# Kernel tuning notes

Hardware: AMD Instinct MI355X
Metric: run time of the kernel (lower is better)

## Reference

```python
import jax, jax.numpy as jnp
import numpy as np

D_MODEL = 4096
D_LATENT = 512
NUM_HEADS = 32
HEAD_DIM = D_MODEL // NUM_HEADS  # 128
ROPE_THETA = 10000.0
BATCH, SEQ = 2, 2048


def _rotate_half(x):
    x1, x2 = jnp.split(x, 2, axis=-1)
    return jnp.concatenate([-x2, x1], axis=-1)


def _rope_cos_sin(positions, head_dim, theta, dtype):
    # positions: [B, S] -> cos/sin: [B, S, 1, head_dim]
    inv_freq = 1.0 / (theta ** (jnp.arange(0, head_dim, 2, dtype=jnp.float32) / head_dim))
    freqs = positions.astype(jnp.float32)[..., None] * inv_freq  # [B,S,hd/2]
    emb = jnp.concatenate([freqs, freqs], axis=-1)               # [B,S,hd]
    return jnp.cos(emb)[:, :, None, :].astype(dtype), jnp.sin(emb)[:, :, None, :].astype(dtype)


def setup_inputs() -> dict:
    key = jax.random.key(0)
    ks = jax.random.split(key, 6)
    s = 0.02
    return {
        "hidden_states": jax.random.normal(ks[0], (BATCH, SEQ, D_MODEL), jnp.float32),
        "Wq": jax.random.normal(ks[1], (D_MODEL, NUM_HEADS * HEAD_DIM), jnp.float32) * s,
        "Wc": jax.random.normal(ks[2], (D_MODEL, D_LATENT), jnp.float32) * s,
        "Wk": jax.random.normal(ks[3], (D_LATENT, NUM_HEADS * HEAD_DIM), jnp.float32) * s,
        "Wv": jax.random.normal(ks[4], (D_LATENT, NUM_HEADS * HEAD_DIM), jnp.float32) * s,
        "Wo": jax.random.normal(ks[5], (NUM_HEADS * HEAD_DIM, D_MODEL), jnp.float32) * s,
    }


def reference(hidden_states, Wq, Wc, Wk, Wv, Wo):
    B, S, _ = hidden_states.shape
    H, Dh = NUM_HEADS, HEAD_DIM

    q = (hidden_states @ Wq).reshape(B, S, H, Dh)
    kv_latent = hidden_states @ Wc                     # [B,S,d_latent]
    k = (kv_latent @ Wk).reshape(B, S, H, Dh)
    v = (kv_latent @ Wv).reshape(B, S, H, Dh)

    # RoPE: q uses positions [0..S), k uses positions [0..S) (no past cache)
    pos = jnp.broadcast_to(jnp.arange(S)[None, :], (B, S))
    cos, sin = _rope_cos_sin(pos, Dh, ROPE_THETA, q.dtype)
    q = q * cos + _rotate_half(q) * sin
    k = k * cos + _rotate_half(k) * sin

    # standard attention, no mask (faithful to attention_mask=None path)
    scale = 1.0 / np.sqrt(Dh)
    scores = jnp.einsum("bqhd,bkhd->bhqk", q, k) * scale
    probs = jax.nn.softmax(scores, axis=-1)
    attn = jnp.einsum("bhqk,bkhd->bqhd", probs, v)     # [B,S,H,Dh]

    out = attn.reshape(B, S, H * Dh) @ Wo
    return out
```

## Files before the change

kernel.cpp:

```cpp
#include <hip/hip_runtime.h>
#include <hip/hip_bf16.h>
#include <cstdint>
#include <cstddef>

#define D_MODEL 4096
#define D_LATENT 512
#define NUM_HEADS 32
#define HEAD_DIM 128
#define BATCH 2
#define SEQ 2048
#define ROWS (BATCH*SEQ)

typedef __attribute__((ext_vector_type(8))) short bf16x8;
typedef __attribute__((ext_vector_type(4))) float f32x4;
typedef __attribute__((ext_vector_type(16))) float f32x16;
typedef unsigned int uint;

static __device__ __forceinline__ unsigned short f2bf(float f){
  union { float f; uint32_t u; } v; v.f = f;
  uint32_t r = (v.u + 0x7fffu + ((v.u >> 16) & 1u)) >> 16;
  return (unsigned short)r;
}
static __device__ __forceinline__ float bf2f(unsigned short h){
  union { uint32_t u; float f; } v; v.u = ((uint32_t)h) << 16;
  return v.f;
}
static __device__ __forceinline__ uint cvtpk(float lo, float hi2){
  uint r;
  asm("v_cvt_pk_bf16_f32 %0, %1, %2" : "=v"(r) : "v"(lo), "v"(hi2));
  return r;
}
static __device__ __forceinline__ void gload16(const void* g, void* l){
  __builtin_amdgcn_global_load_lds(
      (const __attribute__((address_space(1))) void*)g,
      (__attribute__((address_space(3))) void*)l, 16, 0, 0);
}

__global__ __launch_bounds__(256) void f32_to_bf16(
    const float* __restrict__ in, unsigned short* __restrict__ out){
  const size_t i = ((size_t)blockIdx.x * 256 + threadIdx.x) * 8;
  const float4 lo = *(const float4*)(in + i);
  const float4 hi = *(const float4*)(in + i + 4);
  uint4 d; unsigned short* dp = (unsigned short*)&d;
  dp[0]=f2bf(lo.x); dp[1]=f2bf(lo.y); dp[2]=f2bf(lo.z); dp[3]=f2bf(lo.w);
  dp[4]=f2bf(hi.x); dp[5]=f2bf(hi.y); dp[6]=f2bf(hi.z); dp[7]=f2bf(hi.w);
  *(uint4*)(out + i) = d;
}

__global__ __launch_bounds__(256) void transpose_convert(
    const float* __restrict__ W, unsigned short* __restrict__ Wt, int K, int N){
  __shared__ float tile[64][65];
  const int k0 = blockIdx.x * 64, n0 = blockIdx.y * 64;
  const int t = threadIdx.x;
  #pragma unroll
  for (int j = 0; j < 16; ++j){
    const int idx = t + 256*j;
    const int r = idx >> 6, c = idx & 63;
    tile[r][c] = W[(size_t)(k0 + r) * N + n0 + c];
  }
  __syncthreads();
  #pragma unroll
  for (int j = 0; j < 16; ++j){
    const int idx = t + 256*j;
    const int r = idx >> 6, c = idx & 63;
    Wt[(size_t)(n0 + r) * K + k0 + c] = f2bf(tile[c][r]);
  }
}

__global__ __launch_bounds__(256) void v_transpose(
    const unsigned short* __restrict__ v, unsigned short* __restrict__ vt){
  __shared__ unsigned short tile[64][72];
  const int s0 = blockIdx.x * 64, d0 = blockIdx.y * 64, bh = blockIdx.z;
  const int b = bh >> 5, h = bh & 31;
  const int t = threadIdx.x;
  #pragma unroll
  for (int j = 0; j < 2; ++j){
    const int idx = t + 256*j;
    const int r = idx >> 3, ch = idx & 7;
    *(uint4*)&tile[r][ch*8] =
      *(const uint4*)&v[(size_t)(b*SEQ + s0 + r) * D_MODEL + h*128 + d0 + ch*8];
  }
  __syncthreads();
  #pragma unroll
  for (int j = 0; j < 16; ++j){
    const int idx = t + 256*j;
    const int r = idx >> 6, c = idx & 63;
    vt[((size_t)bh*128 + d0 + r) * SEQ + s0 + c] = tile[c][r];
  }
}

__global__ __launch_bounds__(256) void rope_table_kernel(float* __restrict__ ct,
                                                         float* __restrict__ st){
  const int i = blockIdx.x * 256 + threadIdx.x;
  if (i >= SEQ * 64) return;
  const int s = i >> 6, j = i & 63;
  const float inv = powf(10000.0f, -(float)j / 64.0f);
  const double a = (double)s * (double)inv;
  ct[i] = (float)cos(a);
  st[i] = (float)sin(a);
}

__global__ __launch_bounds__(256) void rope_apply(unsigned short* __restrict__ buf,
    const float* __restrict__ ct, const float* __restrict__ st, float scale){
  const int i = blockIdx.x * 256 + threadIdx.x;
  const int j = i & 63;
  const int tmp = i >> 6;
  const int h = tmp & 31;
  const int row = tmp >> 5;
  const int s = row & (SEQ - 1);
  const float c = ct[s*64 + j], sn = st[s*64 + j];
  const size_t base = (size_t)row * D_MODEL + (size_t)h * 128;
  const float x1 = bf2f(buf[base + j]);
  const float x2 = bf2f(buf[base + j + 64]);
  buf[base + j]      = f2bf((x1 * c - x2 * sn) * scale);
  buf[base + j + 64] = f2bf((x2 * c + x1 * sn) * scale);
}

template<bool OF32>
__global__ __launch_bounds__(256) void gemm_kernel(
    const unsigned short* __restrict__ A, const unsigned short* __restrict__ Bt,
    void* __restrict__ Cp, int M, int N, int K){
  __shared__ __align__(16) char As[128 * 128];
  __shared__ __align__(16) char Bs[128 * 128];
  const int t = threadIdx.x;
  const int m0 = blockIdx.y * 128, n0 = blockIdx.x * 128;
  const int l = t & 63, wid = t >> 6;
  const int wr = wid >> 1, wcn = wid & 1;
  const int lr = l & 15, lg = l >> 4;

  const int srow = l >> 3;
  const int gch  = (l & 7) ^ srow;
  const unsigned short* gA = A  + (size_t)(m0 + wid*32 + srow) * K + gch*8;
  const unsigned short* gB = Bt + (size_t)(n0 + wid*32 + srow) * K + gch*8;
  char* lA = As + wid*4096;
  char* lB = Bs + wid*4096;

  f32x4 acc[4][4];
  #pragma unroll
  for (int i = 0; i < 4; ++i)
    #pragma unroll
    for (int j = 0; j < 4; ++j)
      #pragma unroll
      for (int r = 0; r < 4; ++r) acc[i][j][r] = 0.0f;

  const int kTiles = K >> 6;
  for (int kt = 0; kt < kTiles; ++kt){
    const size_t ko = (size_t)kt << 6;
    #pragma unroll
    for (int i = 0; i < 4; ++i){
      gload16(gA + (size_t)i*8*K + ko, lA + i*1024);
      gload16(gB + (size_t)i*8*K + ko, lB + i*1024);
    }
    __syncthreads();
    #pragma unroll
    for (int kc = 0; kc < 2; ++kc){
      bf16x8 af[4], bfv[4];
      const int ch = kc*4 + lg;
      #pragma unroll
      for (int mb = 0; mb < 4; ++mb){
        const int row = wr*64 + mb*16 + lr;
        af[mb] = *(const bf16x8*)(As + row*128 + ((ch ^ (row & 7)) * 16));
      }
      #pragma unroll
      for (int nb = 0; nb < 4; ++nb){
        const int row = wcn*64 + nb*16 + lr;
        bfv[nb] = *(const bf16x8*)(Bs + row*128 + ((ch ^ (row & 7)) * 16));
      }
      #pragma unroll
      for (int mb = 0; mb < 4; ++mb)
        #pragma unroll
        for (int nb = 0; nb < 4; ++nb)
          acc[mb][nb] = __builtin_amdgcn_mfma_f32_16x16x32_bf16(af[mb], bfv[nb], acc[mb][nb], 0, 0, 0);
    }
    __syncthreads();
  }
  #pragma unroll
  for (int mb = 0; mb < 4; ++mb)
    #pragma unroll
    for (int nb = 0; nb < 4; ++nb)
      #pragma unroll
      for (int r = 0; r < 4; ++r){
        const int row = m0 + wr*64 + mb*16 + lg*4 + r;
        const int col = n0 + wcn*64 + nb*16 + lr;
        if constexpr (OF32) ((float*)Cp)[(size_t)row * N + col] = acc[mb][nb][r];
        else ((unsigned short*)Cp)[(size_t)row * N + col] = f2bf(acc[mb][nb][r]);
      }
}

template<int MH>
static __device__ __forceinline__ void rdAh(bf16x8 (&a_)[4][2], const char* buf,
                                            int wr, int lr, int lg){
  #pragma unroll
  for (int mm = 0; mm < 4; ++mm)
    #pragma unroll
    for (int kc = 0; kc < 2; ++kc){
      const int row = wr*128 + (MH*4 + mm)*16 + lr;
      const int ch = kc*4 + lg;
      a_[mm][kc] = *(const bf16x8*)(buf + row*128 + ((ch ^ (row & 7)) * 16));
    }
}
template<int NH>
static __device__ __forceinline__ void rdBh(bf16x8 (&b_)[2][2][2], const char* buf,
                                            int wc, int lr, int lg){
  #pragma unroll
  for (int nn = 0; nn < 2; ++nn)
    #pragma unroll
    for (int kc = 0; kc < 2; ++kc){
      const int row = wc*64 + (NH*2 + nn)*16 + lr;
      const int ch = kc*4 + lg;
      b_[NH][nn][kc] = *(const bf16x8*)(buf + row*128 + ((ch ^ (row & 7)) * 16));
    }
}
template<int MH, int NH>
static __device__ __forceinline__ void mfq(f32x4 (&acc)[8][4],
    const bf16x8 (&a_)[4][2], const bf16x8 (&b_)[2][2][2]){
  __builtin_amdgcn_s_setprio(1);
  #pragma unroll
  for (int kc = 0; kc < 2; ++kc)
    #pragma unroll
    for (int mm = 0; mm < 4; ++mm)
      #pragma unroll
      for (int nn = 0; nn < 2; ++nn)
        acc[MH*4+mm][NH*2+nn] = __builtin_amdgcn_mfma_f32_16x16x32_bf16(
            a_[mm][kc], b_[NH][nn][kc], acc[MH*4+mm][NH*2+nn], 0, 0, 0);
  __builtin_amdgcn_s_setprio(0);
}

#define G256_BAR  __builtin_amdgcn_s_barrier()
#define G256_LGK0 do{ asm volatile("s_waitcnt lgkmcnt(0)" ::: "memory"); \
                      __builtin_amdgcn_sched_barrier(0); }while(0)
#define G256_VM(n) asm volatile("s_waitcnt vmcnt(" #n ")" ::: "memory")

template<bool OF32>
__global__ __launch_bounds__(512, 2) void gemm256_kernel(
    const unsigned short* __restrict__ A, const unsigned short* __restrict__ Bt,
    void* __restrict__ Cp, void* __restrict__ Cp2, int nsplit, int ldc,
    int M, int N, int K){
  __shared__ __align__(16) char lds[131072];
  char* const As0 = lds;
  char* const As1 = lds + 32768;
  char* const Bs0 = lds + 65536;
  char* const Bs1 = lds + 98304;

  const int t = threadIdx.x;
  const int l = t & 63, wid = t >> 6;
  const int wr = wid >> 2, wc = wid & 3;
  const int lr = l & 15, lg = l >> 4;
  const int m0 = blockIdx.y * 256, n0 = blockIdx.x * 256;

  const int srow = t >> 3;
  const int pch = t & 7;
  const int gch = pch ^ (srow & 7);
  const unsigned short* gAb = A  + (size_t)(m0 + srow) * K + gch*8;
  const unsigned short* gBb = Bt + (size_t)(n0 + srow) * K + gch*8;
  const int ldso = srow*128 + pch*16;

  auto stA = [&](char* dst, int half, int kcol){
    const unsigned short* g = gAb + (size_t)half*128*K + kcol;
    gload16(g,                dst + half*16384 + ldso);
    gload16(g + (size_t)64*K, dst + half*16384 + 8192 + ldso);
  };
  auto stB = [&](char* dst, int half, int kcol){
    const unsigned short* g = gBb + (size_t)half*128*K + kcol;
    gload16(g,                dst + half*16384 + ldso);
    gload16(g + (size_t)64*K, dst + half*16384 + 8192 + ldso);
  };

  f32x4 acc[8][4];
  #pragma unroll
  for (int m = 0; m < 8; ++m)
    #pragma unroll
    for (int n = 0; n < 4; ++n)
      #pragma unroll
      for (int r = 0; r < 4; ++r) acc[m][n][r] = 0.0f;
  bf16x8 a_[4][2];
  bf16x8 b_[2][2][2];

  const int niter = K >> 7;
  stA(As0, 0, 0); stA(As0, 1, 0); stB(Bs0, 0, 0); stB(Bs0, 1, 0);
  stA(As1, 0, 64);
  G256_VM(2);
  G256_BAR;
  __builtin_amdgcn_sched_barrier(0);

  for (int j = 0; j < niter; ++j){
    const int k0 = j << 7;
    const bool more = (j + 1 < niter);
    rdAh<0>(a_, As0, wr, lr, lg);
    rdBh<0>(b_, Bs0, wc, lr, lg);
    stA(As1, 1, k0 + 64);
    G256_BAR; G256_LGK0;
    mfq<0,0>(acc, a_, b_);
    G256_BAR;
    rdBh<1>(b_, Bs0, wc, lr, lg);
    stB(Bs1, 0, k0 + 64);
    G256_BAR; G256_LGK0;
    mfq<0,1>(acc, a_, b_);
    G256_BAR;
    rdAh<1>(a_, As0, wr, lr, lg);
    stB(Bs1, 1, k0 + 64);
    G256_BAR; G256_LGK0;
    mfq<1,0>(acc, a_, b_);
    G256_BAR;
    if (more){ stA(As0, 0, k0 + 128); G256_VM(2); }
    else     { G256_VM(0); }
    G256_BAR;
    __builtin_amdgcn_sched_barrier(0);
    mfq<1,1>(acc, a_, b_);
    G256_BAR;
    rdAh<0>(a_, As1, wr, lr, lg);
    rdBh<0>(b_, Bs1, wc, lr, lg);
    if (more) stA(As0, 1, k0 + 128);
    G256_BAR; G256_LGK0;
    mfq<0,0>(acc, a_, b_);
    G256_BAR;
    rdBh<1>(b_, Bs1, wc, lr, lg);
    if (more) stB(Bs0, 0, k0 + 128);
    G256_BAR; G256_LGK0;
    mfq<0,1>(acc, a_, b_);
    G256_BAR;
    rdAh<1>(a_, As1, wr, lr, lg);
    if (more) stB(Bs0, 1, k0 + 128);
    G256_BAR; G256_LGK0;
    mfq<1,0>(acc, a_, b_);
    G256_BAR;
    if (more){ stA(As1, 0, k0 + 192); G256_VM(2); }
    G256_BAR;
    __builtin_amdgcn_sched_barrier(0);
    mfq<1,1>(acc, a_, b_);
    G256_BAR;
  }

  void* outp = Cp;
  int c0 = n0;
  if (n0 >= nsplit){ outp = Cp2; c0 = n0 - nsplit; }
  #pragma unroll
  for (int m = 0; m < 8; ++m)
    #pragma unroll
    for (int n = 0; n < 4; ++n)
      #pragma unroll
      for (int r = 0; r < 4; ++r){
        const int row = m0 + wr*128 + m*16 + lg*4 + r;
        const int col = c0 + wc*64 + n*16 + lr;
        if constexpr (OF32) ((float*)outp)[(size_t)row * ldc + col] = acc[m][n][r];
        else ((unsigned short*)outp)[(size_t)row * ldc + col] = f2bf(acc[m][n][r]);
      }
}

__global__ __launch_bounds__(512) void attn_kernel(
    const unsigned short* __restrict__ q, const unsigned short* __restrict__ kp,
    const unsigned short* __restrict__ vt, const float* __restrict__ ct,
    const float* __restrict__ st, unsigned short* __restrict__ o){
  __shared__ __align__(16) char Ks[2 * 16384];
  __shared__ __align__(16) char Vs[2 * 16384];
  const int t = threadIdx.x;
  const int l = t & 63, w = t >> 6;
  const int lq = l & 31, hi = l >> 5;
  const int bh = blockIdx.x, qb = blockIdx.y;
  const int b = bh >> 5;
  const size_t qbase = (size_t)b * SEQ + qb*256 + w*32;
  const size_t cb = (size_t)(bh & 31) * 128;

  auto stageK = [&](int buf, int kb){
    const size_t kr0 = (size_t)b * SEQ + (size_t)kb*64;
    char* kdst = Ks + buf*16384 + w*2048;
    #pragma unroll
    for (int i = 0; i < 2; ++i){
      const int r = w*8 + i*4 + (l >> 4);
      const int g = (l & 15) ^ (r & 7);
      gload16(kp + (kr0 + r) * D_MODEL + cb + g*8, kdst + i*1024);
    }
  };
  auto stageV = [&](int buf, int kb){
    char* vdst = Vs + buf*16384 + w*2048;
    #pragma unroll
    for (int i = 0; i < 2; ++i){
      const int r = w*16 + i*8 + (l >> 3);
      const int g = (l & 7) ^ (r & 7);
      gload16(vt + ((size_t)bh*128 + r) * SEQ + (size_t)kb*64 + g*8, vdst + i*1024);
    }
  };

  bf16x8 qf[8];
  #pragma unroll
  for (int dc = 0; dc < 8; ++dc)
    qf[dc] = *(const bf16x8*)(q + (qbase + lq) * D_MODEL + cb + dc*16 + hi*8);
  {
    const float qsc = 0.08838834764831845f * 1.4426950408889634f;
    const int s = qb*256 + w*32 + lq;
    #pragma unroll
    for (int dc = 0; dc < 4; ++dc){
      const int j0 = dc*16 + hi*8;
      const float4 c0 = *(const float4*)(ct + s*64 + j0);
      const float4 c1 = *(const float4*)(ct + s*64 + j0 + 4);
      const float4 s0_ = *(const float4*)(st + s*64 + j0);
      const float4 s1_ = *(const float4*)(st + s*64 + j0 + 4);
      const float cc[8] = {c0.x,c0.y,c0.z,c0.w,c1.x,c1.y,c1.z,c1.w};
      const float ss[8] = {s0_.x,s0_.y,s0_.z,s0_.w,s1_.x,s1_.y,s1_.z,s1_.w};
      #pragma unroll
      for (int e = 0; e < 8; ++e){
        const float x1 = bf2f((unsigned short)qf[dc][e]);
        const float x2 = bf2f((unsigned short)qf[dc + 4][e]);
        qf[dc][e]     = (short)f2bf((x1 * cc[e] - x2 * ss[e]) * qsc);
        qf[dc + 4][e] = (short)f2bf((x2 * cc[e] + x1 * ss[e]) * qsc);
      }
    }
  }

  f32x16 O[4];
  #pragma unroll
  for (int nb = 0; nb < 4; ++nb)
    #pragma unroll
    for (int r = 0; r < 16; ++r) O[nb][r] = 0.0f;
  float m = -1e30f, lsum = 0.0f;
  bf16x8 pa[4];

  stageK(0, 0); stageV(0, 0);

  for (int kb = 0; kb < SEQ/64; ++kb){
    const bool more = (kb + 1 < SEQ/64);
    if (more){
      stageK((kb + 1) & 1, kb + 1);
      asm volatile("s_waitcnt vmcnt(4)" ::: "memory");
    } else {
      asm volatile("s_waitcnt vmcnt(2)" ::: "memory");
    }
    __builtin_amdgcn_s_barrier();
    __builtin_amdgcn_sched_barrier(0);
    const char* Kb = Ks + (kb & 1)*16384;

    f32x16 s0, s1;
    #pragma unroll
    for (int r = 0; r < 16; ++r){ s0[r] = 0.0f; s1[r] = 0.0f; }
    __builtin_amdgcn_s_setprio(1);
    #pragma unroll
    for (int dc = 0; dc < 8; ++dc){
      const int ch = dc*2 + hi;
      const bf16x8 k0 = *(const bf16x8*)(Kb + lq*256 + ((ch ^ (lq & 7)) * 16));
      const bf16x8 k1 = *(const bf16x8*)(Kb + (32 + lq)*256 + ((ch ^ (lq & 7)) * 16));
      s0 = __builtin_amdgcn_mfma_f32_32x32x16_bf16(k0, qf[dc], s0, 0, 0, 0);
      s1 = __builtin_amdgcn_mfma_f32_32x32x16_bf16(k1, qf[dc], s1, 0, 0, 0);
    }
    if (kb > 0){
      const char* Vp = Vs + ((kb + 1) & 1)*16384;
      #pragma unroll
      for (int c = 0; c < 4; ++c){
        const int ch = c*2 + hi;
        #pragma unroll
        for (int nb = 0; nb < 4; ++nb){
          const int vr = nb*32 + lq;
          const bf16x8 vf = *(const bf16x8*)(Vp + vr*128 + ((ch ^ (vr & 7)) * 16));
          O[nb] = __builtin_amdgcn_mfma_f32_32x32x16_bf16(pa[c], vf, O[nb], 0, 0, 0);
        }
      }
    }
    __builtin_amdgcn_s_setprio(0);
    __builtin_amdgcn_s_barrier();
    __builtin_amdgcn_sched_barrier(0);
    if (more) stageV((kb + 1) & 1, kb + 1);

    float mt = s0[0];
    #pragma unroll
    for (int r = 1; r < 16; ++r) mt = fmaxf(mt, s0[r]);
    #pragma unroll
    for (int r = 0; r < 16; ++r) mt = fmaxf(mt, s1[r]);
    mt = fmaxf(mt, __shfl_xor(mt, 32));

    if (!__all(mt <= m + 8.0f)){
      const float mnew = fmaxf(m, mt);
      const float al = __builtin_amdgcn_exp2f(m - mnew);
      m = mnew;
      lsum *= al;
      #pragma unroll
      for (int r = 0; r < 16; ++r){
        const int crow = (r & 3) + 8*(r >> 2) + 4*hi;
        const float albr = __shfl(al, crow);
        #pragma unroll
        for (int nb = 0; nb < 4; ++nb) O[nb][r] *= albr;
      }
    }

    float E[32];
    float sum = 0.0f;
    #pragma unroll
    for (int r = 0; r < 16; ++r){ E[r] = __builtin_amdgcn_exp2f(s0[r] - m); sum += E[r]; }
    #pragma unroll
    for (int r = 0; r < 16; ++r){ E[16 + r] = __builtin_amdgcn_exp2f(s1[r] - m); sum += E[16 + r]; }
    sum += __shfl_xor(sum, 32);
    lsum += sum;

    #pragma unroll
    for (int c = 0; c < 4; ++c){
      const int rb = c * 8;
      const uint a_ = cvtpk(E[rb + 0], E[rb + 1]);
      const uint b_ = cvtpk(E[rb + 2], E[rb + 3]);
      const uint c_ = cvtpk(E[rb + 4], E[rb + 5]);
      const uint d_ = cvtpk(E[rb + 6], E[rb + 7]);
      const uint sa = (uint)__shfl_xor((int)a_, 32);
      const uint sb = (uint)__shfl_xor((int)b_, 32);
      const uint sc = (uint)__shfl_xor((int)c_, 32);
      const uint sd = (uint)__shfl_xor((int)d_, 32);
      union { uint u[4]; bf16x8 v; } uu;
      uu.u[0] = hi ? sc : a_;
      uu.u[1] = hi ? sd : b_;
      uu.u[2] = hi ? c_ : sa;
      uu.u[3] = hi ? d_ : sb;
      pa[c] = uu.v;
    }
  }

  asm volatile("s_waitcnt vmcnt(0)" ::: "memory");
  __builtin_amdgcn_s_barrier();
  __builtin_amdgcn_sched_barrier(0);
  {
    const char* Vp = Vs + ((SEQ/64 - 1) & 1)*16384;
    #pragma unroll
    for (int c = 0; c < 4; ++c){
      const int ch = c*2 + hi;
      #pragma unroll
      for (int nb = 0; nb < 4; ++nb){
        const int vr = nb*32 + lq;
        const bf16x8 vf = *(const bf16x8*)(Vp + vr*128 + ((ch ^ (vr & 7)) * 16));
        O[nb] = __builtin_amdgcn_mfma_f32_32x32x16_bf16(pa[c], vf, O[nb], 0, 0, 0);
      }
    }
  }

  const float rinv = 1.0f / lsum;
  #pragma unroll
  for (int r = 0; r < 16; ++r){
    const int crow = (r & 3) + 8*(r >> 2) + 4*hi;
    const float rb_ = __shfl(rinv, crow);
    #pragma unroll
    for (int nb = 0; nb < 4; ++nb)
      o[(qbase + crow) * D_MODEL + cb + nb*32 + lq] = f2bf(O[nb][r] * rb_);
  }
}

extern "C" void kernel_launch(void* const* d_in, const int* in_sizes, int n_in,
                              void* d_out, int out_size, void* d_ws, size_t ws_size,
                              hipStream_t stream){
  const float* hidden = (const float*)d_in[0];
  const float* Wq = (const float*)d_in[1];
  const float* Wc = (const float*)d_in[2];
  const float* Wk = (const float*)d_in[3];
  const float* Wv = (const float*)d_in[4];
  const float* Wo = (const float*)d_in[5];
  float* out = (float*)d_out;

  char* ws = (char*)d_ws;
  size_t off = 0;
  auto alloc = [&](size_t bytes)->char*{
    char* p = ws + off; off += (bytes + 255) & ~(size_t)255; return p;
  };
  unsigned short* Wqt  = (unsigned short*)alloc((size_t)D_MODEL * D_MODEL * 2);
  unsigned short* Wct  = (unsigned short*)alloc((size_t)D_LATENT * D_MODEL * 2);
  unsigned short* Wkvt = (unsigned short*)alloc((size_t)2 * D_MODEL * D_LATENT * 2);
  unsigned short* Wot  = (unsigned short*)alloc((size_t)D_MODEL * D_MODEL * 2);
  unsigned short* latent = (unsigned short*)alloc((size_t)ROWS * D_LATENT * 2);
  unsigned short* qbuf = (unsigned short*)alloc((size_t)ROWS * D_MODEL * 2);
  unsigned short* kbuf = (unsigned short*)alloc((size_t)ROWS * D_MODEL * 2);
  unsigned short* vbuf = (unsigned short*)alloc((size_t)ROWS * D_MODEL * 2);
  unsigned short* attnb= (unsigned short*)alloc((size_t)ROWS * D_MODEL * 2);
  float* ctab = (float*)alloc((size_t)SEQ * 64 * 4);
  float* stab = (float*)alloc((size_t)SEQ * 64 * 4);
  unsigned short* hbf   = attnb;
  unsigned short* vtbuf = Wqt;

  const dim3 B256(256);

  f32_to_bf16<<<(ROWS*(size_t)D_MODEL)/2048, B256, 0, stream>>>(hidden, hbf);
  transpose_convert<<<dim3(64, 64), B256, 0, stream>>>(Wq, Wqt, D_MODEL, D_MODEL);
  transpose_convert<<<dim3(64, 8),  B256, 0, stream>>>(Wc, Wct, D_MODEL, D_LATENT);
  transpose_convert<<<dim3(8, 64),  B256, 0, stream>>>(Wk, Wkvt, D_LATENT, D_MODEL);
  transpose_convert<<<dim3(8, 64),  B256, 0, stream>>>(Wv, Wkvt + (size_t)D_MODEL*D_LATENT, D_LATENT, D_MODEL);
  transpose_convert<<<dim3(64, 64), B256, 0, stream>>>(Wo, Wot, D_MODEL, D_MODEL);
  rope_table_kernel<<<512, B256, 0, stream>>>(ctab, stab);

  gemm_kernel<false><<<dim3(D_LATENT/128, ROWS/128), B256, 0, stream>>>(hbf, Wct, latent, ROWS, D_LATENT, D_MODEL);
  gemm256_kernel<false><<<dim3(D_MODEL/256, ROWS/256), dim3(512), 0, stream>>>(
      hbf, Wqt, qbuf, qbuf, 1 << 30, D_MODEL, ROWS, D_MODEL, D_MODEL);
  gemm256_kernel<false><<<dim3(2*D_MODEL/256, ROWS/256), dim3(512), 0, stream>>>(
      latent, Wkvt, kbuf, vbuf, D_MODEL, D_MODEL, ROWS, 2*D_MODEL, D_LATENT);

  v_transpose<<<dim3(SEQ/64, HEAD_DIM/64, BATCH*NUM_HEADS), B256, 0, stream>>>(vbuf, vtbuf);

  rope_apply<<<(ROWS * NUM_HEADS * 64) / 256, B256, 0, stream>>>(kbuf, ctab, stab, 1.0f);

  attn_kernel<<<dim3(BATCH * NUM_HEADS, SEQ/256), dim3(512), 0, stream>>>(
      qbuf, kbuf, vtbuf, ctab, stab, attnb);

  gemm256_kernel<true><<<dim3(D_MODEL/256, ROWS/256), dim3(512), 0, stream>>>(
      attnb, Wot, out, out, 1 << 30, D_MODEL, ROWS, D_MODEL, D_MODEL);
}
```

Before: 639.7 us.

## Un-skew attention pipeline: compute PV in same iteration, widen K swizzle

Replaces the software-pipelined schedule, where the PV MFMA for tile kb-1 overlapped with QK for tile kb and V staging was split across two barriers, with a simpler loop. Each iteration now waits for all loads, issues K and V prefetch for the next tile together, then runs QK, softmax and PV for the current tile. The K LDS swizzle is widened from 3 to 4 bits to cut bank conflicts on the 256-byte K rows. This drops one barrier per iteration but loses the overlap of PV MFMAs with softmax work and waits on vmcnt(0), which may expose load latency.

Measured after the change: 642.4 us. About the same (+0.4%).

```diff
diff --git a/kernel.cpp b/kernel.cpp
--- a/kernel.cpp
+++ b/kernel.cpp
@@ -367,7 +367,7 @@
     #pragma unroll
     for (int i = 0; i < 2; ++i){
       const int r = w*8 + i*4 + (l >> 4);
-      const int g = (l & 15) ^ (r & 7);
+      const int g = (l & 15) ^ (r & 15);
       gload16(kp + (kr0 + r) * D_MODEL + cb + g*8, kdst + i*1024);
     }
   };
@@ -413,21 +413,17 @@
     #pragma unroll
     for (int r = 0; r < 16; ++r) O[nb][r] = 0.0f;
   float m = -1e30f, lsum = 0.0f;
-  bf16x8 pa[4];
 
   stageK(0, 0); stageV(0, 0);
 
   for (int kb = 0; kb < SEQ/64; ++kb){
     const bool more = (kb + 1 < SEQ/64);
-    if (more){
-      stageK((kb + 1) & 1, kb + 1);
-      asm volatile("s_waitcnt vmcnt(4)" ::: "memory");
-    } else {
-      asm volatile("s_waitcnt vmcnt(2)" ::: "memory");
-    }
+    asm volatile("s_waitcnt vmcnt(0)" ::: "memory");
     __builtin_amdgcn_s_barrier();
     __builtin_amdgcn_sched_barrier(0);
+    if (more){ stageK((kb + 1) & 1, kb + 1); stageV((kb + 1) & 1, kb + 1); }
     const char* Kb = Ks + (kb & 1)*16384;
+    const char* Vb = Vs + (kb & 1)*16384;
 
     f32x16 s0, s1;
     #pragma unroll
@@ -436,28 +432,12 @@
     #pragma unroll
     for (int dc = 0; dc < 8; ++dc){
       const int ch = dc*2 + hi;
-      const bf16x8 k0 = *(const bf16x8*)(Kb + lq*256 + ((ch ^ (lq & 7)) * 16));
-      const bf16x8 k1 = *(const bf16x8*)(Kb + (32 + lq)*256 + ((ch ^ (lq & 7)) * 16));
+      const bf16x8 k0 = *(const bf16x8*)(Kb + lq*256 + ((ch ^ (lq & 15)) * 16));
+      const bf16x8 k1 = *(const bf16x8*)(Kb + (32 + lq)*256 + ((ch ^ (lq & 15)) * 16));
       s0 = __builtin_amdgcn_mfma_f32_32x32x16_bf16(k0, qf[dc], s0, 0, 0, 0);
       s1 = __builtin_amdgcn_mfma_f32_32x32x16_bf16(k1, qf[dc], s1, 0, 0, 0);
     }
-    if (kb > 0){
-      const char* Vp = Vs + ((kb + 1) & 1)*16384;
-      #pragma unroll
-      for (int c = 0; c < 4; ++c){
-        const int ch = c*2 + hi;
-        #pragma unroll
-        for (int nb = 0; nb < 4; ++nb){
-          const int vr = nb*32 + lq;
-          const bf16x8 vf = *(const bf16x8*)(Vp + vr*128 + ((ch ^ (vr & 7)) * 16));
-          O[nb] = __builtin_amdgcn_mfma_f32_32x32x16_bf16(pa[c], vf, O[nb], 0, 0, 0);
-        }
-      }
-    }
     __builtin_amdgcn_s_setprio(0);
-    __builtin_amdgcn_s_barrier();
-    __builtin_amdgcn_sched_barrier(0);
-    if (more) stageV((kb + 1) & 1, kb + 1);
 
     float mt = s0[0];
     #pragma unroll
@@ -489,6 +469,7 @@
     sum += __shfl_xor(sum, 32);
     lsum += sum;
 
+    bf16x8 pa[4];
     #pragma unroll
     for (int c = 0; c < 4; ++c){
       const int rb = c * 8;
@@ -507,23 +488,19 @@
       uu.u[3] = hi ? d_ : sb;
       pa[c] = uu.v;
     }
-  }
-
-  asm volatile("s_waitcnt vmcnt(0)" ::: "memory");
-  __builtin_amdgcn_s_barrier();
-  __builtin_amdgcn_sched_barrier(0);
-  {
-    const char* Vp = Vs + ((SEQ/64 - 1) & 1)*16384;
+
+    __builtin_amdgcn_s_setprio(1);
     #pragma unroll
     for (int c = 0; c < 4; ++c){
       const int ch = c*2 + hi;
       #pragma unroll
       for (int nb = 0; nb < 4; ++nb){
         const int vr = nb*32 + lq;
-        const bf16x8 vf = *(const bf16x8*)(Vp + vr*128 + ((ch ^ (vr & 7)) * 16));
+        const bf16x8 vf = *(const bf16x8*)(Vb + vr*128 + ((ch ^ (vr & 7)) * 16));
         O[nb] = __builtin_amdgcn_mfma_f32_32x32x16_bf16(pa[c], vf, O[nb], 0, 0, 0);
       }
     }
+    __builtin_amdgcn_s_setprio(0);
   }
 
   const float rinv = 1.0f / lsum;
```
